# Kernel tuning notes

Hardware: AMD Instinct MI355X
Metric: run time of the kernel (lower is better)

The kernel has to match this reference:

```python
import jax, jax.numpy as jnp
import numpy as np

N_NODES = 40000
N_EDGES = 640000
D = 128
D_OUT = 128


def setup_inputs() -> dict:
    key = jax.random.key(0)
    k1, k2, k3, k4, k5 = jax.random.split(key, 5)
    x = jax.random.normal(k1, (N_NODES, D), dtype=jnp.float32)
    edge_index = jax.random.randint(k2, (2, N_EDGES), 0, N_NODES, dtype=jnp.int64)
    edge_weight = jax.random.uniform(k3, (N_EDGES,), dtype=jnp.float32)
    W = jax.random.normal(k4, (D_OUT, 2 * D), dtype=jnp.float32) / np.sqrt(2 * D)
    b = jax.random.normal(k5, (D_OUT,), dtype=jnp.float32) * 0.01
    return {"x": x, "edge_index": edge_index, "edge_weight": edge_weight, "W": W, "b": b}


def reference(x, edge_index, edge_weight, W, b):
    src, dst = edge_index[0], edge_index[1]
    n_dst = x.shape[0]
    # gather source features per edge: [E, D]
    msgs = x[src]
    # per-destination weight sums (degree-normalization denominator)
    w_sum = jax.ops.segment_sum(edge_weight, dst, num_segments=n_dst)
    w_norm = edge_weight / jnp.clip(w_sum[dst], 1e-8, None)
    # weighted scatter-add aggregation: [N, D]
    agg = jax.ops.segment_sum(w_norm[:, None] * msgs, dst, num_segments=n_dst)
    # concat self + aggregated neighbors, project
    h = jnp.concatenate([x, agg], axis=-1)
    return h @ W.T + b
```

## Files before the change

### kernel.cpp

```cpp
#include <hip/hip_runtime.h>

constexpr int NN = 40000;
constexpr int NE = 640000;
constexpr int NBKT = 625;
constexpr int CBLK = 128;

typedef __attribute__((ext_vector_type(8))) short short8;
typedef __attribute__((ext_vector_type(4))) float f32x4;

__device__ __forceinline__ unsigned short rneb(float f) {
    unsigned u = __float_as_uint(f);
    u = (u + 0x7FFFu + ((u >> 16) & 1u)) >> 16;
    return (unsigned short)u;
}
__device__ __forceinline__ float b2f(unsigned short s) {
    return __uint_as_float(((unsigned)s) << 16);
}

__global__ __launch_bounds__(1024) void prep_k(const float* __restrict__ x,
                                               unsigned short* __restrict__ xb,
                                               const float* __restrict__ W,
                                               unsigned short* __restrict__ Wb,
                                               const int* __restrict__ dst,
                                               int* __restrict__ gcnt2) {
    __shared__ int cnt[NBKT];
    int bid = blockIdx.x, t = threadIdx.x;
    if (bid < 1250) {
        int g = bid * 1024 + t;
        float4 v = reinterpret_cast<const float4*>(x)[g];
        ushort4 o = { rneb(v.x), rneb(v.y), rneb(v.z), rneb(v.w) };
        reinterpret_cast<ushort4*>(xb)[g] = o;
    } else if (bid < 1258) {
        int g = (bid - 1250) * 1024 + t;
        float4 v = reinterpret_cast<const float4*>(W)[g];
        ushort4 o = { rneb(v.x), rneb(v.y), rneb(v.z), rneb(v.w) };
        reinterpret_cast<ushort4*>(Wb)[g] = o;
    } else {
        int cb = bid - 1258;
        if (t < NBKT) cnt[t] = 0;
        __syncthreads();
        int eb = cb * 5000;
        for (int i = t; i < 5000; i += 1024)
            atomicAdd(&cnt[dst[eb + i] >> 6], 1);
        __syncthreads();
        if (t < NBKT) gcnt2[cb * 640 + t] = cnt[t];
    }
}

__global__ __launch_bounds__(1024) void cscan_k(const int* __restrict__ gcnt2,
                                                int* __restrict__ bptr,
                                                int* __restrict__ cursor) {
    __shared__ int sc[1024];
    int t = threadIdx.x;
    int c = 0;
    if (t < NBKT)
        for (int b = 0; b < CBLK; ++b) c += gcnt2[b * 640 + t];
    sc[t] = c;
    __syncthreads();
    for (int o = 1; o < 1024; o <<= 1) {
        int u = (t >= o) ? sc[t - o] : 0;
        __syncthreads();
        sc[t] += u;
        __syncthreads();
    }
    if (t < NBKT) {
        int excl = sc[t] - c;
        bptr[t]   = excl;
        cursor[t] = excl;
    }
    if (t == 0) bptr[NBKT] = NE;
}

__global__ __launch_bounds__(1024) void cscatter_k(const int* __restrict__ dst,
                                                   const int* __restrict__ src,
                                                   const float* __restrict__ ew,
                                                   int* __restrict__ cursor,
                                                   unsigned* __restrict__ rec,
                                                   unsigned char* __restrict__ dloc) {
    __shared__ int cnt[NBKT];
    __shared__ int base[NBKT];
    int t = threadIdx.x;
    if (t < NBKT) cnt[t] = 0;
    __syncthreads();
    int eb = blockIdx.x * 5000;
    for (int i = t; i < 5000; i += 1024)
        atomicAdd(&cnt[dst[eb + i] >> 6], 1);
    __syncthreads();
    if (t < NBKT) {
        base[t] = atomicAdd(&cursor[t], cnt[t]);
        cnt[t]  = 0;
    }
    __syncthreads();
    for (int i = t; i < 5000; i += 1024) {
        int d   = dst[eb + i];
        int bkt = d >> 6;
        int slot = atomicAdd(&cnt[bkt], 1);
        int p = base[bkt] + slot;
        unsigned short wh = __builtin_bit_cast(unsigned short, (_Float16)ew[eb + i]);
        rec[p]  = (unsigned)src[eb + i] | ((unsigned)wh << 16);
        dloc[p] = (unsigned char)(d & 63);
    }
}

__global__ __launch_bounds__(1024) void aggemm_k(const unsigned* __restrict__ rec,
                                                 const unsigned char* __restrict__ dloc,
                                                 const int* __restrict__ bptr,
                                                 const unsigned short* __restrict__ xb,
                                                 const unsigned short* __restrict__ Wb,
                                                 const float* __restrict__ bias_p,
                                                 float* __restrict__ out) {
    constexpr int CAP = 2048;
    __shared__ unsigned grec[CAP];
    __shared__ int cnt[64];
    __shared__ int cur[64];
    __shared__ int pL[65];
    __shared__ unsigned short hbl[64 * 128];
    int bkt = blockIdx.x, t = threadIdx.x;
    int beg = bptr[bkt], end = bptr[bkt + 1];
    int grp = t >> 4, fl = t & 15;
    const short8* xv = reinterpret_cast<const short8*>(xb);
    float acc[8] = {0.f, 0.f, 0.f, 0.f, 0.f, 0.f, 0.f, 0.f};
    float wsv = 0.f;

    for (int cb = beg; cb < end; cb += CAP) {
        int m = end - cb; if (m > CAP) m = CAP;
        if (t < 64) cnt[t] = 0;
        __syncthreads();
        unsigned r0 = 0, r1 = 0; int d0 = -1, d1 = -1;
        if (t < m)        { r0 = rec[cb + t];        d0 = dloc[cb + t];        atomicAdd(&cnt[d0], 1); }
        if (t + 1024 < m) { r1 = rec[cb + t + 1024]; d1 = dloc[cb + t + 1024]; atomicAdd(&cnt[d1], 1); }
        __syncthreads();
        if (t < 64) {
            int v = cnt[t], s = v;
            #pragma unroll
            for (int o = 1; o < 64; o <<= 1) {
                int u = __shfl_up(s, o);
                if (t >= o) s += u;
            }
            pL[t]  = s - v;
            cur[t] = s - v;
            if (t == 63) pL[64] = s;
        }
        __syncthreads();
        if (d0 >= 0) { int p = atomicAdd(&cur[d0], 1); grec[p] = r0; }
        if (d1 >= 0) { int p = atomicAdd(&cur[d1], 1); grec[p] = r1; }
        __syncthreads();
        int gb = pL[grp], ge = pL[grp + 1];
        int e = gb;
        for (; e + 4 <= ge; e += 4) {
            unsigned q0 = grec[e], q1 = grec[e + 1], q2 = grec[e + 2], q3 = grec[e + 3];
            short8 v0 = xv[(size_t)(q0 & 0xFFFF) * 16 + fl];
            short8 v1 = xv[(size_t)(q1 & 0xFFFF) * 16 + fl];
            short8 v2 = xv[(size_t)(q2 & 0xFFFF) * 16 + fl];
            short8 v3 = xv[(size_t)(q3 & 0xFFFF) * 16 + fl];
            float w0 = (float)__builtin_bit_cast(_Float16, (unsigned short)(q0 >> 16));
            float w1 = (float)__builtin_bit_cast(_Float16, (unsigned short)(q1 >> 16));
            float w2 = (float)__builtin_bit_cast(_Float16, (unsigned short)(q2 >> 16));
            float w3 = (float)__builtin_bit_cast(_Float16, (unsigned short)(q3 >> 16));
            wsv += w0 + w1 + w2 + w3;
            #pragma unroll
            for (int i = 0; i < 8; ++i)
                acc[i] += w0 * b2f((unsigned short)v0[i]) + w1 * b2f((unsigned short)v1[i])
                        + w2 * b2f((unsigned short)v2[i]) + w3 * b2f((unsigned short)v3[i]);
        }
        for (; e < ge; ++e) {
            unsigned q = grec[e];
            short8 v = xv[(size_t)(q & 0xFFFF) * 16 + fl];
            float w = (float)__builtin_bit_cast(_Float16, (unsigned short)(q >> 16));
            wsv += w;
            #pragma unroll
            for (int i = 0; i < 8; ++i) acc[i] += w * b2f((unsigned short)v[i]);
        }
        __syncthreads();
    }

    {
        float inv = 1.f / fmaxf(wsv, 1e-8f);
        short8 o;
        #pragma unroll
        for (int i = 0; i < 8; ++i) o[i] = (short)rneb(acc[i] * inv);
        int gs = fl ^ (grp & 7);
        *reinterpret_cast<short8*>(&hbl[grp * 128 + gs * 8]) = o;
    }
    __syncthreads();

    int w = t >> 6, l = t & 63;
    int l15 = l & 15, lg = l >> 4;
    int rt = w & 3, ct0 = w >> 2;
    f32x4 acc2[2] = { (f32x4)0.f, (f32x4)0.f };
    float bias2[2] = { bias_p[ct0 * 16 + l15], bias_p[(ct0 + 4) * 16 + l15] };
    int arow = bkt * 64 + rt * 16 + l15;

    #pragma unroll
    for (int step = 0; step < 8; ++step) {
        short8 a;
        if (step < 4) {
            a = *reinterpret_cast<const short8*>(xb + (size_t)arow * 128 + step * 32 + lg * 8);
        } else {
            int r = rt * 16 + l15;
            int g = (step - 4) * 4 + lg;
            a = *reinterpret_cast<const short8*>(&hbl[r * 128 + (g ^ (r & 7)) * 8]);
        }
        #pragma unroll
        for (int q = 0; q < 2; ++q) {
            int ct = ct0 + q * 4;
            short8 bf = *reinterpret_cast<const short8*>(Wb + (size_t)(ct * 16 + l15) * 256 + step * 32 + lg * 8);
            acc2[q] = __builtin_amdgcn_mfma_f32_16x16x32_bf16(a, bf, acc2[q], 0, 0, 0);
        }
    }

    #pragma unroll
    for (int q = 0; q < 2; ++q)
        #pragma unroll
        for (int r4 = 0; r4 < 4; ++r4) {
            int row = bkt * 64 + rt * 16 + lg * 4 + r4;
            out[(size_t)row * 128 + (ct0 + q * 4) * 16 + l15] = acc2[q][r4] + bias2[q];
        }
}


__global__ void wsum_k(const int* __restrict__ dst, const float* __restrict__ ew,
                       float* __restrict__ wsum) {
    int e = blockIdx.x * 256 + threadIdx.x;
    if (e < NE) atomicAdd(&wsum[dst[e]], ew[e]);
}

__global__ void zerof_k(float* __restrict__ p, int n4) {
    int g = blockIdx.x * 256 + threadIdx.x;
    if (g < n4) reinterpret_cast<float4*>(p)[g] = make_float4(0.f, 0.f, 0.f, 0.f);
}

__global__ void scatter_k(const int* __restrict__ src, const int* __restrict__ dst,
                          const float* __restrict__ ew, const float* __restrict__ wsum,
                          const float* __restrict__ x, float* __restrict__ agg) {
    int tid = blockIdx.x * 256 + threadIdx.x;
    int e = tid >> 5;
    int p = tid & 31;
    if (e >= NE) return;
    int s = src[e], dn = dst[e];
    float wn = ew[e] / fmaxf(wsum[dn], 1e-8f);
    float4 v = *reinterpret_cast<const float4*>(x + (size_t)s * 128 + p * 4);
    float* o = agg + (size_t)dn * 128 + p * 4;
    atomicAdd(o + 0, wn * v.x);
    atomicAdd(o + 1, wn * v.y);
    atomicAdd(o + 2, wn * v.z);
    atomicAdd(o + 3, wn * v.w);
}

__global__ __launch_bounds__(256) void gemm_f32_k(const float* __restrict__ x,
                                                  const float* __restrict__ agg,
                                                  const float* __restrict__ W,
                                                  const float* __restrict__ b,
                                                  float* __restrict__ out) {
    __shared__ float4 Wl[128 * 64];
    __shared__ float4 hl[16 * 64];
    int t = threadIdx.x;
    int base = blockIdx.x * 80;
    const float4* Wg = reinterpret_cast<const float4*>(W);
    #pragma unroll
    for (int i = 0; i < 32; ++i) {
        int f = t + i * 256;
        int r = f >> 6, kk = f & 63;
        Wl[r * 64 + (kk ^ (r & 7))] = Wg[f];
    }
    int jj = t & 63, wsl = t >> 6, sw = jj & 7;
    float bv[2] = { b[jj], b[jj + 64] };
    const float4* xg = reinterpret_cast<const float4*>(x);
    const float4* ag = reinterpret_cast<const float4*>(agg);
    for (int g = 0; g < 5; ++g) {
        int nbase = base + g * 16;
        __syncthreads();
        #pragma unroll
        for (int i = 0; i < 4; ++i) {
            int f = t + i * 256;
            int ln = f >> 6, kk = f & 63;
            size_t node = (size_t)(nbase + ln);
            hl[ln * 64 + kk] = (kk < 32) ? xg[node * 32 + kk] : ag[node * 32 + (kk - 32)];
        }
        __syncthreads();
        float acc[2][4];
        #pragma unroll
        for (int q = 0; q < 2; ++q)
            #pragma unroll
            for (int n = 0; n < 4; ++n) acc[q][n] = 0.f;
        #pragma unroll 4
        for (int kk = 0; kk < 64; ++kk) {
            float4 h[4];
            #pragma unroll
            for (int n = 0; n < 4; ++n) h[n] = hl[(wsl + 4 * n) * 64 + kk];
            #pragma unroll
            for (int q = 0; q < 2; ++q) {
                float4 wv = Wl[(jj + q * 64) * 64 + (kk ^ sw)];
                #pragma unroll
                for (int n = 0; n < 4; ++n)
                    acc[q][n] += wv.x * h[n].x + wv.y * h[n].y + wv.z * h[n].z + wv.w * h[n].w;
            }
        }
        #pragma unroll
        for (int q = 0; q < 2; ++q)
            #pragma unroll
            for (int n = 0; n < 4; ++n)
                out[(size_t)(nbase + wsl + 4 * n) * 128 + jj + q * 64] = acc[q][n] + bv[q];
    }
}

extern "C" void kernel_launch(void* const* d_in, const int* in_sizes, int n_in,
                              void* d_out, int out_size, void* d_ws, size_t ws_size,
                              hipStream_t stream) {
    const float* x  = (const float*)d_in[0];
    const int*   ei = (const int*)d_in[1];
    const float* ew = (const float*)d_in[2];
    const float* W  = (const float*)d_in[3];
    const float* b  = (const float*)d_in[4];
    float* out = (float*)d_out;
    const int* src = ei;
    const int* dst = ei + NE;

    const size_t off_cursor = 4096;
    const size_t off_gcnt2  = 8192;
    const size_t off_Wb     = 339968;
    const size_t off_dloc   = 405504;
    const size_t off_rec    = 1048576;
    const size_t off_xb     = 3670016;
    const size_t need = off_xb + (size_t)NN * 128 * 2;

    if (ws_size >= need) {
        int* bptr   = (int*)d_ws;
        int* cursor = (int*)((char*)d_ws + off_cursor);
        int* gcnt2  = (int*)((char*)d_ws + off_gcnt2);
        unsigned short* Wb = (unsigned short*)((char*)d_ws + off_Wb);
        unsigned char* dloc = (unsigned char*)((char*)d_ws + off_dloc);
        unsigned* rec = (unsigned*)((char*)d_ws + off_rec);
        unsigned short* xb = (unsigned short*)((char*)d_ws + off_xb);

        prep_k    <<<1386, 1024, 0, stream>>>(x, xb, W, Wb, dst, gcnt2);
        cscan_k   <<<1, 1024, 0, stream>>>(gcnt2, bptr, cursor);
        cscatter_k<<<CBLK, 1024, 0, stream>>>(dst, src, ew, cursor, rec, dloc);
        aggemm_k  <<<NBKT, 1024, 0, stream>>>(rec, dloc, bptr, xb, Wb, b, out);
    } else {
        float* wsum = (float*)d_ws;
        float* agg  = out;
        zerof_k  <<<(NN / 4 + 255) / 256, 256, 0, stream>>>(wsum, NN / 4);
        zerof_k  <<<(NN * 32 + 255) / 256, 256, 0, stream>>>(agg, NN * 32);
        wsum_k   <<<(NE + 255) / 256, 256, 0, stream>>>(dst, ew, wsum);
        scatter_k<<<NE * 32 / 256, 256, 0, stream>>>(src, dst, ew, wsum, x, agg);
        gemm_f32_k<<<500, 256, 0, stream>>>(x, agg, W, b, out);
    }
}
```

Before: 91.07 us.

## Gather neighbor features in FP8 and reuse per-block bucket counts in scatter

Adds an FP8 (e4m3) copy of x, written during prep, and has the aggregation gather read 8 bytes per lane instead of 16. This halves the random-gather traffic in the neighbor aggregation. The scatter kernel now reuses the per-block bucket counts from prep instead of recounting destinations, which removes one pass over dst. The cost is lower precision in the aggregated features, which risks failing accuracy tolerance, plus an extra 5 MB write in prep.

```diff
diff --git a/kernel.cpp b/kernel.cpp
--- a/kernel.cpp
+++ b/kernel.cpp
@@ -7,6 +7,7 @@
 
 typedef __attribute__((ext_vector_type(8))) short short8;
 typedef __attribute__((ext_vector_type(4))) float f32x4;
+typedef __attribute__((ext_vector_type(2))) float f32x2;
 
 __device__ __forceinline__ unsigned short rneb(float f) {
     unsigned u = __float_as_uint(f);
@@ -17,8 +18,65 @@
     return __uint_as_float(((unsigned)s) << 16);
 }
 
+#if defined(__has_builtin)
+#if __has_builtin(__builtin_amdgcn_cvt_pk_f32_fp8) && __has_builtin(__builtin_amdgcn_cvt_pk_fp8_f32)
+#define FP8_HW 1
+#endif
+#endif
+
+#ifndef FP8_HW
+__device__ __forceinline__ unsigned char f32_to_fp8_sw(float f) {
+    float a = fabsf(f);
+    unsigned s = (f < 0.f) ? 0x80u : 0u;
+    if (a > 448.f) a = 448.f;
+    unsigned char r;
+    if (a < 0.015625f) {
+        int m = (int)rintf(a * 512.f);
+        r = (m >= 8) ? (unsigned char)0x08 : (unsigned char)m;
+    } else {
+        unsigned u = __float_as_uint(a);
+        u += 0x0007FFFFu + ((u >> 20) & 1u);
+        int e8 = (int)((u >> 23) & 0xFF) - 127 + 7;
+        unsigned m = (u >> 20) & 7u;
+        if (e8 > 15 || (e8 == 15 && m == 7)) { e8 = 15; m = 6; }
+        r = (unsigned char)((e8 << 3) | m);
+    }
+    return r | (unsigned char)s;
+}
+__device__ __forceinline__ float fp8_to_f32_sw(unsigned char b) {
+    unsigned s = (b >> 7) & 1u, e = (b >> 3) & 0xFu, m = b & 7u;
+    float v = e ? ldexpf((float)(8 + m), (int)e - 10) : ldexpf((float)m, -9);
+    return s ? -v : v;
+}
+#endif
+
+__device__ __forceinline__ unsigned pack_fp8x4(float4 v) {
+#ifdef FP8_HW
+    unsigned r = __builtin_amdgcn_cvt_pk_fp8_f32(v.x, v.y, 0, false);
+    r = __builtin_amdgcn_cvt_pk_fp8_f32(v.z, v.w, (int)r, true);
+    return r;
+#else
+    return (unsigned)f32_to_fp8_sw(v.x) | ((unsigned)f32_to_fp8_sw(v.y) << 8)
+         | ((unsigned)f32_to_fp8_sw(v.z) << 16) | ((unsigned)f32_to_fp8_sw(v.w) << 24);
+#endif
+}
+
+__device__ __forceinline__ void unpack_fp8x4(unsigned u, float* o) {
+#ifdef FP8_HW
+    f32x2 d0 = __builtin_amdgcn_cvt_pk_f32_fp8(u, false);
+    f32x2 d1 = __builtin_amdgcn_cvt_pk_f32_fp8(u, true);
+    o[0] = d0[0]; o[1] = d0[1]; o[2] = d1[0]; o[3] = d1[1];
+#else
+    o[0] = fp8_to_f32_sw((unsigned char)(u & 0xFF));
+    o[1] = fp8_to_f32_sw((unsigned char)((u >> 8) & 0xFF));
+    o[2] = fp8_to_f32_sw((unsigned char)((u >> 16) & 0xFF));
+    o[3] = fp8_to_f32_sw((unsigned char)((u >> 24) & 0xFF));
+#endif
+}
+
 __global__ __launch_bounds__(1024) void prep_k(const float* __restrict__ x,
                                                unsigned short* __restrict__ xb,
+                                               unsigned* __restrict__ x8w,
                                                const float* __restrict__ W,
                                                unsigned short* __restrict__ Wb,
                                                const int* __restrict__ dst,
@@ -30,6 +88,7 @@
         float4 v = reinterpret_cast<const float4*>(x)[g];
         ushort4 o = { rneb(v.x), rneb(v.y), rneb(v.z), rneb(v.w) };
         reinterpret_cast<ushort4*>(xb)[g] = o;
+        x8w[g] = pack_fp8x4(v);
     } else if (bid < 1258) {
         int g = (bid - 1250) * 1024 + t;
         float4 v = reinterpret_cast<const float4*>(W)[g];
@@ -74,23 +133,21 @@
 __global__ __launch_bounds__(1024) void cscatter_k(const int* __restrict__ dst,
                                                    const int* __restrict__ src,
                                                    const float* __restrict__ ew,
+                                                   const int* __restrict__ gcnt2,
                                                    int* __restrict__ cursor,
                                                    unsigned* __restrict__ rec,
                                                    unsigned char* __restrict__ dloc) {
     __shared__ int cnt[NBKT];
     __shared__ int base[NBKT];
     int t = threadIdx.x;
-    if (t < NBKT) cnt[t] = 0;
+    int cb = blockIdx.x;
+    if (t < NBKT) {
+        int c = gcnt2[cb * 640 + t];
+        base[t] = c ? atomicAdd(&cursor[t], c) : 0;
+        cnt[t] = 0;
+    }
     __syncthreads();
-    int eb = blockIdx.x * 5000;
-    for (int i = t; i < 5000; i += 1024)
-        atomicAdd(&cnt[dst[eb + i] >> 6], 1);
-    __syncthreads();
-    if (t < NBKT) {
-        base[t] = atomicAdd(&cursor[t], cnt[t]);
-        cnt[t]  = 0;
-    }
-    __syncthreads();
+    int eb = cb * 5000;
     for (int i = t; i < 5000; i += 1024) {
         int d   = dst[eb + i];
         int bkt = d >> 6;
@@ -106,6 +163,7 @@
                                                  const unsigned char* __restrict__ dloc,
                                                  const int* __restrict__ bptr,
                                                  const unsigned short* __restrict__ xb,
+                                                 const unsigned char* __restrict__ x8,
                                                  const unsigned short* __restrict__ Wb,
                                                  const float* __restrict__ bias_p,
                                                  float* __restrict__ out) {
@@ -118,7 +176,7 @@
     int bkt = blockIdx.x, t = threadIdx.x;
     int beg = bptr[bkt], end = bptr[bkt + 1];
     int grp = t >> 4, fl = t & 15;
-    const short8* xv = reinterpret_cast<const short8*>(xb);
+    const uint2* xv = reinterpret_cast<const uint2*>(x8);
     float acc[8] = {0.f, 0.f, 0.f, 0.f, 0.f, 0.f, 0.f, 0.f};
     float wsv = 0.f;
 
@@ -149,27 +207,38 @@
         int e = gb;
         for (; e + 4 <= ge; e += 4) {
             unsigned q0 = grec[e], q1 = grec[e + 1], q2 = grec[e + 2], q3 = grec[e + 3];
-            short8 v0 = xv[(size_t)(q0 & 0xFFFF) * 16 + fl];
-            short8 v1 = xv[(size_t)(q1 & 0xFFFF) * 16 + fl];
-            short8 v2 = xv[(size_t)(q2 & 0xFFFF) * 16 + fl];
-            short8 v3 = xv[(size_t)(q3 & 0xFFFF) * 16 + fl];
+            uint2 a0 = xv[(size_t)(q0 & 0xFFFF) * 16 + fl];
+            uint2 a1 = xv[(size_t)(q1 & 0xFFFF) * 16 + fl];
+            uint2 a2 = xv[(size_t)(q2 & 0xFFFF) * 16 + fl];
+            uint2 a3 = xv[(size_t)(q3 & 0xFFFF) * 16 + fl];
             float w0 = (float)__builtin_bit_cast(_Float16, (unsigned short)(q0 >> 16));
             float w1 = (float)__builtin_bit_cast(_Float16, (unsigned short)(q1 >> 16));
             float w2 = (float)__builtin_bit_cast(_Float16, (unsigned short)(q2 >> 16));
             float w3 = (float)__builtin_bit_cast(_Float16, (unsigned short)(q3 >> 16));
             wsv += w0 + w1 + w2 + w3;
-            #pragma unroll
-            for (int i = 0; i < 8; ++i)
-                acc[i] += w0 * b2f((unsigned short)v0[i]) + w1 * b2f((unsigned short)v1[i])
-                        + w2 * b2f((unsigned short)v2[i]) + w3 * b2f((unsigned short)v3[i]);
+            float f[8];
+            unpack_fp8x4(a0.x, f); unpack_fp8x4(a0.y, f + 4);
+            #pragma unroll
+            for (int i = 0; i < 8; ++i) acc[i] += w0 * f[i];
+            unpack_fp8x4(a1.x, f); unpack_fp8x4(a1.y, f + 4);
+            #pragma unroll
+            for (int i = 0; i < 8; ++i) acc[i] += w1 * f[i];
+            unpack_fp8x4(a2.x, f); unpack_fp8x4(a2.y, f + 4);
+            #pragma unroll
+            for (int i = 0; i < 8; ++i) acc[i] += w2 * f[i];
+            unpack_fp8x4(a3.x, f); unpack_fp8x4(a3.y, f + 4);
+            #pragma unroll
+            for (int i = 0; i < 8; ++i) acc[i] += w3 * f[i];
         }
         for (; e < ge; ++e) {
             unsigned q = grec[e];
-            short8 v = xv[(size_t)(q & 0xFFFF) * 16 + fl];
+            uint2 a = xv[(size_t)(q & 0xFFFF) * 16 + fl];
             float w = (float)__builtin_bit_cast(_Float16, (unsigned short)(q >> 16));
             wsv += w;
-            #pragma unroll
-            for (int i = 0; i < 8; ++i) acc[i] += w * b2f((unsigned short)v[i]);
+            float f[8];
+            unpack_fp8x4(a.x, f); unpack_fp8x4(a.y, f + 4);
+            #pragma unroll
+            for (int i = 0; i < 8; ++i) acc[i] += w * f[i];
         }
         __syncthreads();
     }
@@ -290,10 +359,10 @@
             for (int n = 0; n < 4; ++n) h[n] = hl[(wsl + 4 * n) * 64 + kk];
             #pragma unroll
             for (int q = 0; q < 2; ++q) {
-                float4 wv = Wl[(jj + q * 64) * 64 + (kk ^ sw)];
+                float4 wvv = Wl[(jj + q * 64) * 64 + (kk ^ sw)];
                 #pragma unroll
                 for (int n = 0; n < 4; ++n)
-                    acc[q][n] += wv.x * h[n].x + wv.y * h[n].y + wv.z * h[n].z + wv.w * h[n].w;
+                    acc[q][n] += wvv.x * h[n].x + wvv.y * h[n].y + wvv.z * h[n].z + wvv.w * h[n].w;
             }
         }
         #pragma unroll
@@ -322,7 +391,8 @@
     const size_t off_dloc   = 405504;
     const size_t off_rec    = 1048576;
     const size_t off_xb     = 3670016;
-    const size_t need = off_xb + (size_t)NN * 128 * 2;
+    const size_t off_x8     = 13910016;
+    const size_t need = off_x8 + (size_t)NN * 128;
 
     if (ws_size >= need) {
         int* bptr   = (int*)d_ws;
@@ -332,11 +402,12 @@
         unsigned char* dloc = (unsigned char*)((char*)d_ws + off_dloc);
         unsigned* rec = (unsigned*)((char*)d_ws + off_rec);
         unsigned short* xb = (unsigned short*)((char*)d_ws + off_xb);
-
-        prep_k    <<<1386, 1024, 0, stream>>>(x, xb, W, Wb, dst, gcnt2);
+        unsigned char* x8 = (unsigned char*)((char*)d_ws + off_x8);
+
+        prep_k    <<<1386, 1024, 0, stream>>>(x, xb, (unsigned*)x8, W, Wb, dst, gcnt2);
         cscan_k   <<<1, 1024, 0, stream>>>(gcnt2, bptr, cursor);
-        cscatter_k<<<CBLK, 1024, 0, stream>>>(dst, src, ew, cursor, rec, dloc);
-        aggemm_k  <<<NBKT, 1024, 0, stream>>>(rec, dloc, bptr, xb, Wb, b, out);
+        cscatter_k<<<CBLK, 1024, 0, stream>>>(dst, src, ew, gcnt2, cursor, rec, dloc);
+        aggemm_k  <<<NBKT, 1024, 0, stream>>>(rec, dloc, bptr, xb, x8, Wb, b, out);
     } else {
         float* wsum = (float*)d_ws;
         float* agg  = out;
```

New measurement: 84.38 us. 7.3% less time.
